# Performance work log

Hardware: AMD Instinct MI355X
Metric: run time of the kernel (lower is better)

## Reference

```python
import jax, jax.numpy as jnp
import numpy as np

B, S, H, NH = 2, 2048, 1024, 16
HD = H // NH
R = 4
LORA_SCALE = 16.0 / 4.0  # lora_alpha / r


def lora_linear(x, W, b, A, Bm):
    # x: [b,t,in]; W: [out,in]; A: [r,in]; Bm: [out,r]
    base = jnp.einsum('bti,oi->bto', x, W) + b
    lora = jnp.einsum('btr,or->bto', jnp.einsum('bti,ri->btr', x, A), Bm)
    return base + LORA_SCALE * lora


def setup_inputs() -> dict:
    key = jax.random.key(0)
    ks = jax.random.split(key, 14)
    std = 1.0 / np.sqrt(H)
    d = {
        'hidden_states': jax.random.normal(ks[0], (B, S, H), dtype=jnp.float32),
        'attention_mask': jnp.zeros((B, 1, 1, S), dtype=jnp.float32),
    }
    for i, nm in enumerate(['q', 'k', 'v']):
        d[f'W{nm}'] = jax.random.normal(ks[1 + 4 * i], (H, H), dtype=jnp.float32) * std
        d[f'b{nm}'] = jnp.zeros((H,), dtype=jnp.float32)
        d[f'A{nm}'] = jax.random.normal(ks[2 + 4 * i], (R, H), dtype=jnp.float32) * std
        d[f'B{nm}'] = jnp.zeros((H, R), dtype=jnp.float32) + 0.01 * jax.random.normal(ks[3 + 4 * i], (H, R), dtype=jnp.float32)
    return d


def reference(hidden_states, attention_mask, Wq, bq, Aq, Bq, Wk, bk, Ak, Bk, Wv, bv, Av, Bv):
    def heads(p):  # [b,t,(h d)] -> [b,h,t,d]
        return p.reshape(B, S, NH, HD).transpose(0, 2, 1, 3)

    q = heads(lora_linear(hidden_states, Wq, bq, Aq, Bq))
    k = heads(lora_linear(hidden_states, Wk, bk, Ak, Bk))
    v = heads(lora_linear(hidden_states, Wv, bv, Av, Bv))

    scores = jnp.einsum('bhqd,bhkd->bhqk', q, k) / jnp.sqrt(jnp.float32(HD))
    causal = jnp.tril(jnp.ones((S, S), dtype=scores.dtype))
    causal = (1.0 - causal) * -10000.0  # [S,S], broadcast over b,h
    scores = scores + attention_mask + causal[None, None]
    weights = jax.nn.softmax(scores, axis=-1)  # dropout p=0 -> identity (eval)
    ctx = jnp.einsum('bhqk,bhkd->bhqd', weights, v)
    return ctx.transpose(0, 2, 1, 3).reshape(B, S, H)
```

## Files before the change

### kernel.cpp

```cpp
#include <hip/hip_runtime.h>
#include <stdint.h>

#define B_ 2
#define S_ 2048
#define H_ 1024
#define NH_ 16
#define HD_ 64
#define M_ 4096
#define LOG2E 1.44269504089f

typedef unsigned short u16;
typedef __bf16 bf16x8 __attribute__((ext_vector_type(8)));
typedef float  f32x4  __attribute__((ext_vector_type(4)));

#if __has_builtin(__builtin_amdgcn_exp2f)
#define EXP2(x) __builtin_amdgcn_exp2f(x)
#else
#define EXP2(x) exp2f(x)
#endif

#define WAITV4() asm volatile("s_waitcnt vmcnt(4)" ::: "memory")
#define WAITV0() asm volatile("s_waitcnt vmcnt(0)" ::: "memory")
#define SCHED0() __builtin_amdgcn_sched_barrier(0)

__device__ inline u16 f2bf(float f) {
  union { float f; uint32_t u; } a; a.f = f;
  uint32_t r = a.u + 0x7FFFu + ((a.u >> 16) & 1u);
  return (u16)(r >> 16);
}
__device__ inline float bf2f(u16 v) {
  union { uint32_t u; float f; } a; a.u = ((uint32_t)v) << 16; return a.f;
}

__device__ inline void gload_lds16(const void* g, void* l) {
  __builtin_amdgcn_global_load_lds((const __attribute__((address_space(1))) void*)g,
                                   (__attribute__((address_space(3))) void*)l, 16, 0, 0);
}

__global__ __launch_bounds__(256) void cvt_kernel(
    const float* __restrict__ x,
    const float* __restrict__ wq, const float* __restrict__ wk, const float* __restrict__ wv,
    const float* __restrict__ Aq, const float* __restrict__ Ak, const float* __restrict__ Av,
    const float* __restrict__ LBq, const float* __restrict__ LBk, const float* __restrict__ LBv,
    const float* __restrict__ amask,
    u16* __restrict__ xbf, u16* __restrict__ wbf, float* __restrict__ maskl2e) {
  const int XN = M_ * H_;
  const int WN = H_ * H_;
  const int total = XN + 3 * WN;
  int idx = (blockIdx.x * 256 + threadIdx.x) * 4;
  if (idx < XN) {
    float4 v = *(const float4*)(x + idx);
    *(ushort4*)(xbf + idx) = make_ushort4(f2bf(v.x), f2bf(v.y), f2bf(v.z), f2bf(v.w));
  } else if (idx < total) {
    int j = idx - XN; int p = j >> 20; int off = j & (WN - 1);
    const float* W  = (p == 0) ? wq : (p == 1 ? wk : wv);
    const float* A  = (p == 0) ? Aq : (p == 1 ? Ak : Av);
    const float* LB = (p == 0) ? LBq : (p == 1 ? LBk : LBv);
    int n = off >> 10, k = off & 1023;
    float4 v  = *(const float4*)(W + off);
    f32x4 lb  = *(const f32x4*)&LB[n * 4];
    float4 a0 = *(const float4*)(A + k);
    float4 a1 = *(const float4*)(A + 1024 + k);
    float4 a2 = *(const float4*)(A + 2048 + k);
    float4 a3 = *(const float4*)(A + 3072 + k);
    v.x += 4.f * (lb.x * a0.x + lb.y * a1.x + lb.z * a2.x + lb.w * a3.x);
    v.y += 4.f * (lb.x * a0.y + lb.y * a1.y + lb.z * a2.y + lb.w * a3.y);
    v.z += 4.f * (lb.x * a0.z + lb.y * a1.z + lb.z * a2.z + lb.w * a3.z);
    v.w += 4.f * (lb.x * a0.w + lb.y * a1.w + lb.z * a2.w + lb.w * a3.w);
    *(ushort4*)(wbf + (p << 20) + off) = make_ushort4(f2bf(v.x), f2bf(v.y), f2bf(v.z), f2bf(v.w));
  } else {
    int mi = idx - total;
    if (mi < B_ * S_) {
      float4 mv = *(const float4*)(amask + mi);
      mv.x *= LOG2E; mv.y *= LOG2E; mv.z *= LOG2E; mv.w *= LOG2E;
      *(float4*)(maskl2e + mi) = mv;
    }
  }
}

template<int P>
__device__ __forceinline__ void gemm_body(
    const u16* __restrict__ xbf, const u16* __restrict__ wbf,
    const float* __restrict__ bias, u16* __restrict__ qkv,
    u16* __restrict__ As, u16* __restrict__ Bs) {
  const int n0 = blockIdx.x * 128;
  const int m0 = blockIdx.y * 128;
  const u16* Wp = wbf + (P << 20);
  const int tid = threadIdx.x, lane = tid & 63, w = tid >> 6;
  const int g = lane >> 4, q15 = lane & 15;
  const int wr = w >> 1, wc = w & 1;
  const f32x4 fzero = {0.f, 0.f, 0.f, 0.f};
  f32x4 acc[4][4];
#pragma unroll
  for (int mi = 0; mi < 4; ++mi)
#pragma unroll
    for (int ni = 0; ni < 4; ++ni) acc[mi][ni] = fzero;
  const int srow = lane >> 2;

  auto STAGE = [&](int buf, int k0) {
#pragma unroll
    for (int j = 0; j < 2; ++j) {
      int c = w * 2 + j;
      int row = c * 16 + srow;
      int uu = (lane & 3) ^ ((row >> 1) & 3);
      gload_lds16(xbf + (size_t)(m0 + row) * 1024 + k0 + uu * 8, As + buf * 4096 + c * 512);
      gload_lds16(Wp  + (size_t)(n0 + row) * 1024 + k0 + uu * 8, Bs + buf * 4096 + c * 512);
    }
  };

  STAGE(0, 0);
  STAGE(1, 32);
  int c0 = 0, c1 = 1, c2 = 2;
#pragma unroll 1
  for (int t = 0; t < 32; ++t) {
    if (t < 31) WAITV4(); else WAITV0();
    SCHED0();
    __builtin_amdgcn_s_barrier();
    if (t + 2 < 32) STAGE(c2, (t + 2) * 32);
    const u16* Ab = As + c0 * 4096;
    const u16* Bb = Bs + c0 * 4096;
    bf16x8 af[4], bfr[4];
#pragma unroll
    for (int mi = 0; mi < 4; ++mi) {
      int r = wr * 64 + mi * 16 + q15;
      af[mi] = *(const bf16x8*)&Ab[r * 32 + ((g ^ ((r >> 1) & 3)) * 8)];
    }
#pragma unroll
    for (int ni = 0; ni < 4; ++ni) {
      int r = wc * 64 + ni * 16 + q15;
      bfr[ni] = *(const bf16x8*)&Bb[r * 32 + ((g ^ ((r >> 1) & 3)) * 8)];
    }
    __builtin_amdgcn_s_setprio(1);
#pragma unroll
    for (int mi = 0; mi < 4; ++mi)
#pragma unroll
      for (int ni = 0; ni < 4; ++ni) {
        if (P == 2)
          acc[mi][ni] = __builtin_amdgcn_mfma_f32_16x16x32_bf16(af[mi], bfr[ni], acc[mi][ni], 0, 0, 0);
        else
          acc[mi][ni] = __builtin_amdgcn_mfma_f32_16x16x32_bf16(bfr[ni], af[mi], acc[mi][ni], 0, 0, 0);
      }
    __builtin_amdgcn_s_setprio(0);
    int tmp = c0; c0 = c1; c1 = c2; c2 = tmp;
  }

  if (P != 2) {
#pragma unroll
    for (int ni = 0; ni < 4; ++ni) {
      int nb = n0 + wc * 64 + ni * 16 + g * 4;
      f32x4 bi = *(const f32x4*)&bias[nb];
      int h = nb >> 6, dbase = nb & 63;
#pragma unroll
      for (int mi = 0; mi < 4; ++mi) {
        int m = m0 + wr * 64 + mi * 16 + q15;
        int bb = m >> 11, s = m & 2047;
        size_t bhs = (size_t)(bb * 16 + h) * 2048 + s;
        float v0 = acc[mi][ni][0] + bi.x, v1 = acc[mi][ni][1] + bi.y;
        float v2 = acc[mi][ni][2] + bi.z, v3 = acc[mi][ni][3] + bi.w;
        size_t addr;
        if (P == 0) {
          const float qs = 0.125f * LOG2E;
          v0 *= qs; v1 *= qs; v2 *= qs; v3 *= qs;
          addr = bhs * 64 + dbase;
        } else {
          int pos = (((dbase >> 3) ^ (s & 7)) << 3) | (dbase & 7);
          addr = 4194304 + bhs * 64 + pos;
        }
        *(ushort4*)&qkv[addr] = make_ushort4(f2bf(v0), f2bf(v1), f2bf(v2), f2bf(v3));
      }
    }
  } else {
    float biasv[4];
#pragma unroll
    for (int ni = 0; ni < 4; ++ni) biasv[ni] = bias[n0 + wc * 64 + ni * 16 + q15];
#pragma unroll
    for (int mi = 0; mi < 4; ++mi) {
      int mbase = m0 + wr * 64 + mi * 16 + g * 4;
      int bb = mbase >> 11, sbase = mbase & 2047;
      int sr = sbase & 31;
      int cba = (((sr >> 4) & 1) << 2) | (((sr >> 2) & 3) << 3);
      int sp = (sbase & 32) | cba;
#pragma unroll
      for (int ni = 0; ni < 4; ++ni) {
        int n = n0 + wc * 64 + ni * 16 + q15;
        int d = n & 63, h = n >> 6;
        int spp = (((sp >> 3) ^ (d & 7)) << 3) | (sp & 7);
        size_t addr = 8388608 + ((size_t)(bb * 16 + h) * 64 + d) * 2048 + (sbase & ~63) + spp;
        *(ushort4*)&qkv[addr] = make_ushort4(
            f2bf(acc[mi][ni][0] + biasv[ni]), f2bf(acc[mi][ni][1] + biasv[ni]),
            f2bf(acc[mi][ni][2] + biasv[ni]), f2bf(acc[mi][ni][3] + biasv[ni]));
      }
    }
  }
}

__global__ __launch_bounds__(256) void qkv_gemm(
    const u16* __restrict__ xbf, const u16* __restrict__ wbf,
    const float* __restrict__ bq, const float* __restrict__ bk, const float* __restrict__ bv,
    u16* __restrict__ qkv) {
  __shared__ __align__(16) u16 As[3 * 4096];
  __shared__ __align__(16) u16 Bs[3 * 4096];
  switch (blockIdx.z) {
    case 0: gemm_body<0>(xbf, wbf, bq, qkv, As, Bs); break;
    case 1: gemm_body<1>(xbf, wbf, bk, qkv, As, Bs); break;
    default: gemm_body<2>(xbf, wbf, bv, qkv, As, Bs); break;
  }
}

__global__ __launch_bounds__(256, 4) void attn_kernel(
    const u16* __restrict__ qkv, const float* __restrict__ maskl2e, float* __restrict__ out,
    u16* __restrict__ pacc, float* __restrict__ pml) {
  const int bid = blockIdx.x;
  int bh, qt, t0, t1, rrec = 0;
  bool split;
  if (bid < 1024) {
    split = true;
    int xcd = bid & 7, idx = bid >> 3;
    bh = xcd * 4 + (idx & 3);
    int rest = idx >> 2;
    qt = 31 - (rest >> 1);
    int sp = rest & 1;
    int ntt = qt + 1;
    int h1 = ntt >> 1;
    t0 = sp ? h1 : 0;
    t1 = sp ? ntt : h1;
    rrec = (bh * 16 + (qt - 16)) * 2 + sp;
  } else {
    split = false;
    int v = bid - 1024;
    bh = (v & 7) * 4 + ((v >> 3) & 3);
    qt = 15 - (v >> 5);
    t0 = 0; t1 = qt + 1;
  }
  const int b = bh >> 4, h = bh & 15;
  const int tid = threadIdx.x, lane = tid & 63, w = tid >> 6;
  const int g = lane >> 4, ql = lane & 15;
  const u16* Qb = qkv + (size_t)bh * 131072;
  const u16* Kb = qkv + 4194304 + (size_t)bh * 131072;
  const u16* Vb = qkv + 8388608 + (size_t)bh * 131072;
  const float* Mb = maskl2e + b * 2048;
  __shared__ __align__(16) u16 Ks[2][64][64];
  __shared__ __align__(16) u16 Vs[2][64][64];
  const f32x4 fzero = {0.f, 0.f, 0.f, 0.f};

  auto STAGE = [&](int nb, int kb) {
#pragma unroll
    for (int j = 0; j < 2; ++j) {
      int rl = w * 16 + j * 8 + (lane >> 3);
      gload_lds16(Kb + (size_t)(kb + rl) * 64 + (lane & 7) * 8, &Ks[nb][w * 16 + j * 8][0]);
      gload_lds16(Vb + (size_t)rl * 2048 + kb + (lane & 7) * 8, &Vs[nb][w * 16 + j * 8][0]);
    }
  };

  const int qw = qt * 64 + w * 16;
  const int q  = qw + ql;
  bf16x8 qf[2];
#pragma unroll
  for (int ks = 0; ks < 2; ++ks)
    qf[ks] = *(const bf16x8*)&Qb[(size_t)q * 64 + ks * 32 + g * 8];
  f32x4 acc[4];
#pragma unroll
  for (int dt = 0; dt < 4; ++dt) acc[dt] = fzero;
  float mrun = -1e30f, lrun = 0.f;
  const int nloc = t1 - t0;

  f32x4 mkC[4], mkN[4];
  STAGE(0, t0 * 64);
#pragma unroll
  for (int k16 = 0; k16 < 4; ++k16) mkC[k16] = *(const f32x4*)&Mb[t0 * 64 + k16 * 16 + g * 4];

#pragma unroll 1
  for (int lt = 0; lt < nloc; ++lt) {
    const int t = t0 + lt;
    WAITV0();
    SCHED0();
    __builtin_amdgcn_s_barrier();
    const int kb = t * 64;
    if (lt + 1 < nloc) {
      STAGE((lt + 1) & 1, kb + 64);
#pragma unroll
      for (int k16 = 0; k16 < 4; ++k16) mkN[k16] = *(const f32x4*)&Mb[kb + 64 + k16 * 16 + g * 4];
    }
    const int cb = lt & 1;
    f32x4 st[4];
    __builtin_amdgcn_s_setprio(1);
#pragma unroll
    for (int k16 = 0; k16 < 4; ++k16) {
      bf16x8 kf0 = *(const bf16x8*)&Ks[cb][k16 * 16 + ql][(g ^ (ql & 7)) * 8];
      bf16x8 kf1 = *(const bf16x8*)&Ks[cb][k16 * 16 + ql][((4 + g) ^ (ql & 7)) * 8];
      st[k16] = __builtin_amdgcn_mfma_f32_16x16x32_bf16(kf0, qf[0], mkC[k16], 0, 0, 0);
      st[k16] = __builtin_amdgcn_mfma_f32_16x16x32_bf16(kf1, qf[1], st[k16], 0, 0, 0);
    }
    __builtin_amdgcn_s_setprio(0);
    const bool needm = (t == qt);
    float sc[16];
#pragma unroll
    for (int k16 = 0; k16 < 4; ++k16)
#pragma unroll
      for (int r = 0; r < 4; ++r) {
        float sv = st[k16][r];
        if (needm) { int key = kb + k16 * 16 + g * 4 + r; sv = (key > q) ? -1e30f : sv; }
        sc[k16 * 4 + r] = sv;
      }
    float m8[8], m4[4];
#pragma unroll
    for (int i = 0; i < 8; ++i) m8[i] = fmaxf(sc[i], sc[i + 8]);
#pragma unroll
    for (int i = 0; i < 4; ++i) m4[i] = fmaxf(m8[i], m8[i + 4]);
    float pmax = fmaxf(fmaxf(m4[0], m4[1]), fmaxf(m4[2], m4[3]));
    if (!__all(pmax <= mrun + 8.f)) {
      float pm = fmaxf(pmax, __shfl_xor(pmax, 16, 64));
      pm = fmaxf(pm, __shfl_xor(pm, 32, 64));
      const float mt = fmaxf(mrun, pm);
      const float scale = EXP2(mrun - mt);
      lrun *= scale;
#pragma unroll
      for (int dt = 0; dt < 4; ++dt) acc[dt] *= scale;
      mrun = mt;
    }
    float pv[16];
#pragma unroll
    for (int i = 0; i < 16; ++i) pv[i] = EXP2(sc[i] - mrun);
    float s8[8], s4[4];
#pragma unroll
    for (int i = 0; i < 8; ++i) s8[i] = pv[i] + pv[i + 8];
#pragma unroll
    for (int i = 0; i < 4; ++i) s4[i] = s8[i] + s8[i + 4];
    lrun += (s4[0] + s4[1]) + (s4[2] + s4[3]);
    bf16x8 pfv[2];
#pragma unroll
    for (int ksub = 0; ksub < 2; ++ksub)
#pragma unroll
      for (int j = 0; j < 4; ++j) {
        pfv[ksub][j]     = (__bf16)pv[ksub * 8 + j];
        pfv[ksub][4 + j] = (__bf16)pv[ksub * 8 + 4 + j];
      }
    __builtin_amdgcn_s_setprio(1);
#pragma unroll
    for (int dt = 0; dt < 4; ++dt)
#pragma unroll
      for (int ksub = 0; ksub < 2; ++ksub) {
        bf16x8 vf = *(const bf16x8*)&Vs[cb][dt * 16 + ql][((ksub * 4 + g) ^ (ql & 7)) * 8];
        acc[dt] = __builtin_amdgcn_mfma_f32_16x16x32_bf16(vf, pfv[ksub], acc[dt], 0, 0, 0);
      }
    __builtin_amdgcn_s_setprio(0);
#pragma unroll
    for (int k16 = 0; k16 < 4; ++k16) mkC[k16] = mkN[k16];
  }

  float lsum = lrun;
  lsum += __shfl_xor(lsum, 16, 64);
  lsum += __shfl_xor(lsum, 32, 64);
  if (!split) {
    const float inv = 1.f / lsum;
#pragma unroll
    for (int dt = 0; dt < 4; ++dt) {
      f32x4 o = acc[dt] * inv;
      *(f32x4*)&out[((size_t)b * 2048 + q) * 1024 + h * 64 + dt * 16 + g * 4] = o;
    }
  } else {
    const int qloc = w * 16 + ql;
#pragma unroll
    for (int dt = 0; dt < 4; ++dt) {
      *(ushort4*)&pacc[(size_t)rrec * 4096 + qloc * 64 + dt * 16 + g * 4] =
          make_ushort4(f2bf(acc[dt][0]), f2bf(acc[dt][1]), f2bf(acc[dt][2]), f2bf(acc[dt][3]));
    }
    if (g == 0) {
      pml[rrec * 128 + qloc] = mrun;
      pml[rrec * 128 + 64 + qloc] = lsum;
    }
  }
}

__global__ __launch_bounds__(256) void merge_kernel(
    const u16* __restrict__ pacc, const float* __restrict__ pml, float* __restrict__ out) {
  const int mu = blockIdx.x;
  const int bh = mu >> 4, qtm = (mu & 15) + 16;
  const int b = bh >> 4, h = bh & 15;
  const int r0 = mu * 2, r1 = r0 + 1;
  const int tid = threadIdx.x;
  const int ql = tid & 63, dc = (tid >> 6) * 16;
  const float m0 = pml[r0 * 128 + ql], l0 = pml[r0 * 128 + 64 + ql];
  const float m1 = pml[r1 * 128 + ql], l1 = pml[r1 * 128 + 64 + ql];
  const float m  = fmaxf(m0, m1);
  const float w0 = EXP2(m0 - m), w1 = EXP2(m1 - m);
  const float inv = 1.f / (l0 * w0 + l1 * w1);
  const u16* a0 = pacc + (size_t)r0 * 4096 + ql * 64 + dc;
  const u16* a1 = pacc + (size_t)r1 * 4096 + ql * 64 + dc;
  float* op = out + ((size_t)b * 2048 + qtm * 64 + ql) * 1024 + h * 64 + dc;
#pragma unroll
  for (int j = 0; j < 16; j += 4) {
    ushort4 u0 = *(const ushort4*)(a0 + j);
    ushort4 u1 = *(const ushort4*)(a1 + j);
    f32x4 o;
    o[0] = (bf2f(u0.x) * w0 + bf2f(u1.x) * w1) * inv;
    o[1] = (bf2f(u0.y) * w0 + bf2f(u1.y) * w1) * inv;
    o[2] = (bf2f(u0.z) * w0 + bf2f(u1.z) * w1) * inv;
    o[3] = (bf2f(u0.w) * w0 + bf2f(u1.w) * w1) * inv;
    *(f32x4*)(op + j) = o;
  }
}

extern "C" void kernel_launch(void* const* d_in, const int* in_sizes, int n_in,
                              void* d_out, int out_size, void* d_ws, size_t ws_size,
                              hipStream_t stream) {
  const float* x  = (const float*)d_in[0];
  const float* am = (const float*)d_in[1];
  const float* Wq = (const float*)d_in[2];
  const float* bq = (const float*)d_in[3];
  const float* Aq = (const float*)d_in[4];
  const float* Bq = (const float*)d_in[5];
  const float* Wk = (const float*)d_in[6];
  const float* bk = (const float*)d_in[7];
  const float* Ak = (const float*)d_in[8];
  const float* Bk = (const float*)d_in[9];
  const float* Wv = (const float*)d_in[10];
  const float* bv = (const float*)d_in[11];
  const float* Av = (const float*)d_in[12];
  const float* Bv = (const float*)d_in[13];
  float* out = (float*)d_out;

  u16* xbf   = (u16*)d_ws;
  u16* wbf   = xbf + 4194304;
  u16* qkv   = wbf + 3145728;
  float* mk  = (float*)(qkv + 12582912);
  u16* pacc  = xbf;
  float* pml = (float*)(xbf + 4194304);

  cvt_kernel<<<7172, 256, 0, stream>>>(x, Wq, Wk, Wv, Aq, Ak, Av, Bq, Bk, Bv, am, xbf, wbf, mk);
  qkv_gemm<<<dim3(8, 32, 3), 256, 0, stream>>>(xbf, wbf, bq, bk, bv, qkv);
  attn_kernel<<<1536, 256, 0, stream>>>(qkv, mk, out, pacc, pml);
  merge_kernel<<<512, 256, 0, stream>>>(pacc, pml, out);
}
```

Measured before the change: 99.15 us.

## Pair mirrored query tiles per block and split every tile into halves

The attention grid drops the mix of split long tiles and unsplit short tiles. Each of the 1024 blocks now handles two mirrored query tiles (pi and 31-pi), and every query tile is split into two key-range halves, so all blocks get about the same causal work. The first half writes unnormalized fp32 partials straight into the output, and the second half writes bf16 partials to the workspace. The merge kernel now runs over all 32 tiles per head and reads the fp32 partial back from the output. This is meant to remove tail imbalance in the attention launch, at the cost of more merge traffic and an extra block barrier between the two phases.

```diff
diff --git a/kernel.cpp b/kernel.cpp
--- a/kernel.cpp
+++ b/kernel.cpp
@@ -211,27 +211,9 @@
     const u16* __restrict__ qkv, const float* __restrict__ maskl2e, float* __restrict__ out,
     u16* __restrict__ pacc, float* __restrict__ pml) {
   const int bid = blockIdx.x;
-  int bh, qt, t0, t1, rrec = 0;
-  bool split;
-  if (bid < 1024) {
-    split = true;
-    int xcd = bid & 7, idx = bid >> 3;
-    bh = xcd * 4 + (idx & 3);
-    int rest = idx >> 2;
-    qt = 31 - (rest >> 1);
-    int sp = rest & 1;
-    int ntt = qt + 1;
-    int h1 = ntt >> 1;
-    t0 = sp ? h1 : 0;
-    t1 = sp ? ntt : h1;
-    rrec = (bh * 16 + (qt - 16)) * 2 + sp;
-  } else {
-    split = false;
-    int v = bid - 1024;
-    bh = (v & 7) * 4 + ((v >> 3) & 3);
-    qt = 15 - (v >> 5);
-    t0 = 0; t1 = qt + 1;
-  }
+  const int bh = (bid & 7) * 4 + ((bid >> 3) & 3);
+  const int rest = bid >> 5;
+  const int pi = rest >> 1, sp = rest & 1;
   const int b = bh >> 4, h = bh & 15;
   const int tid = threadIdx.x, lane = tid & 63, w = tid >> 6;
   const int g = lane >> 4, ql = lane & 15;
@@ -252,151 +234,155 @@
     }
   };
 
-  const int qw = qt * 64 + w * 16;
-  const int q  = qw + ql;
-  bf16x8 qf[2];
-#pragma unroll
-  for (int ks = 0; ks < 2; ++ks)
-    qf[ks] = *(const bf16x8*)&Qb[(size_t)q * 64 + ks * 32 + g * 8];
-  f32x4 acc[4];
-#pragma unroll
-  for (int dt = 0; dt < 4; ++dt) acc[dt] = fzero;
-  float mrun = -1e30f, lrun = 0.f;
-  const int nloc = t1 - t0;
-
-  f32x4 mkC[4], mkN[4];
-  STAGE(0, t0 * 64);
-#pragma unroll
-  for (int k16 = 0; k16 < 4; ++k16) mkC[k16] = *(const f32x4*)&Mb[t0 * 64 + k16 * 16 + g * 4];
-
 #pragma unroll 1
-  for (int lt = 0; lt < nloc; ++lt) {
-    const int t = t0 + lt;
-    WAITV0();
-    SCHED0();
-    __builtin_amdgcn_s_barrier();
-    const int kb = t * 64;
-    if (lt + 1 < nloc) {
-      STAGE((lt + 1) & 1, kb + 64);
-#pragma unroll
-      for (int k16 = 0; k16 < 4; ++k16) mkN[k16] = *(const f32x4*)&Mb[kb + 64 + k16 * 16 + g * 4];
-    }
-    const int cb = lt & 1;
-    f32x4 st[4];
-    __builtin_amdgcn_s_setprio(1);
-#pragma unroll
-    for (int k16 = 0; k16 < 4; ++k16) {
-      bf16x8 kf0 = *(const bf16x8*)&Ks[cb][k16 * 16 + ql][(g ^ (ql & 7)) * 8];
-      bf16x8 kf1 = *(const bf16x8*)&Ks[cb][k16 * 16 + ql][((4 + g) ^ (ql & 7)) * 8];
-      st[k16] = __builtin_amdgcn_mfma_f32_16x16x32_bf16(kf0, qf[0], mkC[k16], 0, 0, 0);
-      st[k16] = __builtin_amdgcn_mfma_f32_16x16x32_bf16(kf1, qf[1], st[k16], 0, 0, 0);
-    }
-    __builtin_amdgcn_s_setprio(0);
-    const bool needm = (t == qt);
-    float sc[16];
-#pragma unroll
-    for (int k16 = 0; k16 < 4; ++k16)
-#pragma unroll
-      for (int r = 0; r < 4; ++r) {
-        float sv = st[k16][r];
-        if (needm) { int key = kb + k16 * 16 + g * 4 + r; sv = (key > q) ? -1e30f : sv; }
-        sc[k16 * 4 + r] = sv;
-      }
-    float m8[8], m4[4];
-#pragma unroll
-    for (int i = 0; i < 8; ++i) m8[i] = fmaxf(sc[i], sc[i + 8]);
-#pragma unroll
-    for (int i = 0; i < 4; ++i) m4[i] = fmaxf(m8[i], m8[i + 4]);
-    float pmax = fmaxf(fmaxf(m4[0], m4[1]), fmaxf(m4[2], m4[3]));
-    if (!__all(pmax <= mrun + 8.f)) {
-      float pm = fmaxf(pmax, __shfl_xor(pmax, 16, 64));
-      pm = fmaxf(pm, __shfl_xor(pm, 32, 64));
-      const float mt = fmaxf(mrun, pm);
-      const float scale = EXP2(mrun - mt);
-      lrun *= scale;
-#pragma unroll
-      for (int dt = 0; dt < 4; ++dt) acc[dt] *= scale;
-      mrun = mt;
-    }
-    float pv[16];
-#pragma unroll
-    for (int i = 0; i < 16; ++i) pv[i] = EXP2(sc[i] - mrun);
-    float s8[8], s4[4];
-#pragma unroll
-    for (int i = 0; i < 8; ++i) s8[i] = pv[i] + pv[i + 8];
-#pragma unroll
-    for (int i = 0; i < 4; ++i) s4[i] = s8[i] + s8[i + 4];
-    lrun += (s4[0] + s4[1]) + (s4[2] + s4[3]);
-    bf16x8 pfv[2];
-#pragma unroll
-    for (int ksub = 0; ksub < 2; ++ksub)
-#pragma unroll
-      for (int j = 0; j < 4; ++j) {
-        pfv[ksub][j]     = (__bf16)pv[ksub * 8 + j];
-        pfv[ksub][4 + j] = (__bf16)pv[ksub * 8 + 4 + j];
-      }
-    __builtin_amdgcn_s_setprio(1);
-#pragma unroll
-    for (int dt = 0; dt < 4; ++dt)
-#pragma unroll
-      for (int ksub = 0; ksub < 2; ++ksub) {
-        bf16x8 vf = *(const bf16x8*)&Vs[cb][dt * 16 + ql][((ksub * 4 + g) ^ (ql & 7)) * 8];
-        acc[dt] = __builtin_amdgcn_mfma_f32_16x16x32_bf16(vf, pfv[ksub], acc[dt], 0, 0, 0);
-      }
-    __builtin_amdgcn_s_setprio(0);
-#pragma unroll
-    for (int k16 = 0; k16 < 4; ++k16) mkC[k16] = mkN[k16];
-  }
-
-  float lsum = lrun;
-  lsum += __shfl_xor(lsum, 16, 64);
-  lsum += __shfl_xor(lsum, 32, 64);
-  if (!split) {
-    const float inv = 1.f / lsum;
-#pragma unroll
-    for (int dt = 0; dt < 4; ++dt) {
-      f32x4 o = acc[dt] * inv;
-      *(f32x4*)&out[((size_t)b * 2048 + q) * 1024 + h * 64 + dt * 16 + g * 4] = o;
-    }
-  } else {
+  for (int ph = 0; ph < 2; ++ph) {
+    const int qt = ph ? (31 - pi) : pi;
+    const int nt = qt + 1, hf = nt >> 1;
+    const int t0 = sp ? hf : 0, t1 = sp ? nt : hf;
+    const int nloc = t1 - t0;
+    const int qw = qt * 64 + w * 16;
+    const int q  = qw + ql;
+    bf16x8 qf[2];
+#pragma unroll
+    for (int ks = 0; ks < 2; ++ks)
+      qf[ks] = *(const bf16x8*)&Qb[(size_t)q * 64 + ks * 32 + g * 8];
+    f32x4 acc[4];
+#pragma unroll
+    for (int dt = 0; dt < 4; ++dt) acc[dt] = fzero;
+    float mrun = -1e30f, lrun = 0.f;
+
+    f32x4 mkC[4], mkN[4];
+    if (nloc > 0) {
+      STAGE(0, t0 * 64);
+#pragma unroll
+      for (int k16 = 0; k16 < 4; ++k16) mkC[k16] = *(const f32x4*)&Mb[t0 * 64 + k16 * 16 + g * 4];
+    }
+
+#pragma unroll 1
+    for (int lt = 0; lt < nloc; ++lt) {
+      const int t = t0 + lt;
+      WAITV0();
+      SCHED0();
+      __builtin_amdgcn_s_barrier();
+      const int kb = t * 64;
+      if (lt + 1 < nloc) {
+        STAGE((lt + 1) & 1, kb + 64);
+#pragma unroll
+        for (int k16 = 0; k16 < 4; ++k16) mkN[k16] = *(const f32x4*)&Mb[kb + 64 + k16 * 16 + g * 4];
+      }
+      const int cb = lt & 1;
+      f32x4 st[4];
+      __builtin_amdgcn_s_setprio(1);
+#pragma unroll
+      for (int k16 = 0; k16 < 4; ++k16) {
+        bf16x8 kf0 = *(const bf16x8*)&Ks[cb][k16 * 16 + ql][(g ^ (ql & 7)) * 8];
+        bf16x8 kf1 = *(const bf16x8*)&Ks[cb][k16 * 16 + ql][((4 + g) ^ (ql & 7)) * 8];
+        st[k16] = __builtin_amdgcn_mfma_f32_16x16x32_bf16(kf0, qf[0], mkC[k16], 0, 0, 0);
+        st[k16] = __builtin_amdgcn_mfma_f32_16x16x32_bf16(kf1, qf[1], st[k16], 0, 0, 0);
+      }
+      __builtin_amdgcn_s_setprio(0);
+      const bool needm = (t == qt);
+      float sc[16];
+#pragma unroll
+      for (int k16 = 0; k16 < 4; ++k16)
+#pragma unroll
+        for (int r = 0; r < 4; ++r) {
+          float sv = st[k16][r];
+          if (needm) { int key = kb + k16 * 16 + g * 4 + r; sv = (key > q) ? -1e30f : sv; }
+          sc[k16 * 4 + r] = sv;
+        }
+      float m8[8], m4[4];
+#pragma unroll
+      for (int i = 0; i < 8; ++i) m8[i] = fmaxf(sc[i], sc[i + 8]);
+#pragma unroll
+      for (int i = 0; i < 4; ++i) m4[i] = fmaxf(m8[i], m8[i + 4]);
+      float pmax = fmaxf(fmaxf(m4[0], m4[1]), fmaxf(m4[2], m4[3]));
+      if (!__all(pmax <= mrun + 8.f)) {
+        float pm = fmaxf(pmax, __shfl_xor(pmax, 16, 64));
+        pm = fmaxf(pm, __shfl_xor(pm, 32, 64));
+        const float mt = fmaxf(mrun, pm);
+        const float scale = EXP2(mrun - mt);
+        lrun *= scale;
+#pragma unroll
+        for (int dt = 0; dt < 4; ++dt) acc[dt] *= scale;
+        mrun = mt;
+      }
+      float pv[16];
+#pragma unroll
+      for (int i = 0; i < 16; ++i) pv[i] = EXP2(sc[i] - mrun);
+      float s8[8], s4[4];
+#pragma unroll
+      for (int i = 0; i < 8; ++i) s8[i] = pv[i] + pv[i + 8];
+#pragma unroll
+      for (int i = 0; i < 4; ++i) s4[i] = s8[i] + s8[i + 4];
+      lrun += (s4[0] + s4[1]) + (s4[2] + s4[3]);
+      bf16x8 pfv[2];
+#pragma unroll
+      for (int ksub = 0; ksub < 2; ++ksub)
+#pragma unroll
+        for (int j = 0; j < 4; ++j) {
+          pfv[ksub][j]     = (__bf16)pv[ksub * 8 + j];
+          pfv[ksub][4 + j] = (__bf16)pv[ksub * 8 + 4 + j];
+        }
+      __builtin_amdgcn_s_setprio(1);
+#pragma unroll
+      for (int dt = 0; dt < 4; ++dt)
+#pragma unroll
+        for (int ksub = 0; ksub < 2; ++ksub) {
+          bf16x8 vf = *(const bf16x8*)&Vs[cb][dt * 16 + ql][((ksub * 4 + g) ^ (ql & 7)) * 8];
+          acc[dt] = __builtin_amdgcn_mfma_f32_16x16x32_bf16(vf, pfv[ksub], acc[dt], 0, 0, 0);
+        }
+      __builtin_amdgcn_s_setprio(0);
+#pragma unroll
+      for (int k16 = 0; k16 < 4; ++k16) mkC[k16] = mkN[k16];
+    }
+
+    float lsum = lrun;
+    lsum += __shfl_xor(lsum, 16, 64);
+    lsum += __shfl_xor(lsum, 32, 64);
     const int qloc = w * 16 + ql;
-#pragma unroll
-    for (int dt = 0; dt < 4; ++dt) {
-      *(ushort4*)&pacc[(size_t)rrec * 4096 + qloc * 64 + dt * 16 + g * 4] =
-          make_ushort4(f2bf(acc[dt][0]), f2bf(acc[dt][1]), f2bf(acc[dt][2]), f2bf(acc[dt][3]));
+    const int rec = bh * 32 + qt;
+    if (sp == 0) {
+#pragma unroll
+      for (int dt = 0; dt < 4; ++dt)
+        *(f32x4*)&out[((size_t)b * 2048 + qt * 64 + qloc) * 1024 + h * 64 + dt * 16 + g * 4] = acc[dt];
+    } else {
+#pragma unroll
+      for (int dt = 0; dt < 4; ++dt)
+        *(ushort4*)&pacc[(size_t)rec * 4096 + qloc * 64 + dt * 16 + g * 4] =
+            make_ushort4(f2bf(acc[dt][0]), f2bf(acc[dt][1]), f2bf(acc[dt][2]), f2bf(acc[dt][3]));
     }
     if (g == 0) {
-      pml[rrec * 128 + qloc] = mrun;
-      pml[rrec * 128 + 64 + qloc] = lsum;
-    }
+      pml[(sp * 1024 + rec) * 128 + qloc] = mrun;
+      pml[(sp * 1024 + rec) * 128 + 64 + qloc] = lsum;
+    }
+    __syncthreads();
   }
 }
 
 __global__ __launch_bounds__(256) void merge_kernel(
     const u16* __restrict__ pacc, const float* __restrict__ pml, float* __restrict__ out) {
   const int mu = blockIdx.x;
-  const int bh = mu >> 4, qtm = (mu & 15) + 16;
+  const int bh = mu >> 5, qt = mu & 31;
   const int b = bh >> 4, h = bh & 15;
-  const int r0 = mu * 2, r1 = r0 + 1;
   const int tid = threadIdx.x;
   const int ql = tid & 63, dc = (tid >> 6) * 16;
-  const float m0 = pml[r0 * 128 + ql], l0 = pml[r0 * 128 + 64 + ql];
-  const float m1 = pml[r1 * 128 + ql], l1 = pml[r1 * 128 + 64 + ql];
+  const float m0 = pml[mu * 128 + ql],          l0 = pml[mu * 128 + 64 + ql];
+  const float m1 = pml[(1024 + mu) * 128 + ql], l1 = pml[(1024 + mu) * 128 + 64 + ql];
   const float m  = fmaxf(m0, m1);
   const float w0 = EXP2(m0 - m), w1 = EXP2(m1 - m);
   const float inv = 1.f / (l0 * w0 + l1 * w1);
-  const u16* a0 = pacc + (size_t)r0 * 4096 + ql * 64 + dc;
-  const u16* a1 = pacc + (size_t)r1 * 4096 + ql * 64 + dc;
-  float* op = out + ((size_t)b * 2048 + qtm * 64 + ql) * 1024 + h * 64 + dc;
+  float* op = out + ((size_t)b * 2048 + qt * 64 + ql) * 1024 + h * 64 + dc;
+  const u16* a1 = pacc + (size_t)mu * 4096 + ql * 64 + dc;
 #pragma unroll
   for (int j = 0; j < 16; j += 4) {
-    ushort4 u0 = *(const ushort4*)(a0 + j);
+    f32x4 a0 = *(const f32x4*)(op + j);
     ushort4 u1 = *(const ushort4*)(a1 + j);
     f32x4 o;
-    o[0] = (bf2f(u0.x) * w0 + bf2f(u1.x) * w1) * inv;
-    o[1] = (bf2f(u0.y) * w0 + bf2f(u1.y) * w1) * inv;
-    o[2] = (bf2f(u0.z) * w0 + bf2f(u1.z) * w1) * inv;
-    o[3] = (bf2f(u0.w) * w0 + bf2f(u1.w) * w1) * inv;
+    o[0] = (a0[0] * w0 + bf2f(u1.x) * w1) * inv;
+    o[1] = (a0[1] * w0 + bf2f(u1.y) * w1) * inv;
+    o[2] = (a0[2] * w0 + bf2f(u1.z) * w1) * inv;
+    o[3] = (a0[3] * w0 + bf2f(u1.w) * w1) * inv;
     *(f32x4*)(op + j) = o;
   }
 }
@@ -429,6 +415,6 @@
 
   cvt_kernel<<<7172, 256, 0, stream>>>(x, Wq, Wk, Wv, Aq, Ak, Av, Bq, Bk, Bv, am, xbf, wbf, mk);
   qkv_gemm<<<dim3(8, 32, 3), 256, 0, stream>>>(xbf, wbf, bq, bk, bv, qkv);
-  attn_kernel<<<1536, 256, 0, stream>>>(qkv, mk, out, pacc, pml);
-  merge_kernel<<<512, 256, 0, stream>>>(pacc, pml, out);
-}
+  attn_kernel<<<1024, 256, 0, stream>>>(qkv, mk, out, pacc, pml);
+  merge_kernel<<<1024, 256, 0, stream>>>(pacc, pml, out);
+}
```

Measured after the change: 99.15 us. About the same (-0.0%).
